# Kernel optimization log

Hardware: AMD Instinct MI355X
Metric: run time of the kernel (lower is better)

## Reference

```python
import jax, jax.numpy as jnp
import numpy as np

B, L, V, D, H, C = 2048, 200, 50000, 300, 128, 20


def setup_inputs() -> dict:
    key = jax.random.key(0)
    k = jax.random.split(key, 7)
    x = jax.random.randint(k[0], (B, L), 0, V)
    lengths = jax.random.randint(k[1], (B,), 1, L + 1)  # avoid div-by-zero
    emb_table = jax.random.normal(k[2], (V, D), dtype=jnp.float32)
    W_new = jax.random.normal(k[3], (H, 2 * D), dtype=jnp.float32) * 0.02
    b_new = jax.random.normal(k[4], (H,), dtype=jnp.float32) * 0.02
    W3 = jax.random.normal(k[5], (C, H), dtype=jnp.float32) * 0.02
    b3 = jax.random.normal(k[6], (C,), dtype=jnp.float32) * 0.02
    return {"x": x, "lengths": lengths, "emb_table": emb_table,
            "W_new": W_new, "b_new": b_new, "W3": W3, "b3": b3}


def reference(x, lengths, emb_table, W_new, b_new, W3, b3):
    # [B, L, D] embedding gather
    emb = emb_table[x]
    len_f = lengths.astype(emb.dtype)[:, None]          # [B, 1]
    s = jnp.sum(emb, axis=1)                            # [B, D]
    mx = jnp.max(emb, axis=1)                           # [B, D] (max over padded length, as in original)
    # Original bug preserved: 'mean' feature is sum / lengths^2 (divided twice)
    mean_bug = s / (len_f * len_f)                      # [B, D]
    rep = jnp.concatenate([mean_bug, mx], axis=-1)      # [B, 2D]
    h = jax.nn.relu(rep @ W_new.T + b_new)              # [B, H]
    logits2 = h @ W3.T + b3                             # [B, C]
    return logits2
```

## Files before the change

### kernel.cpp

```cpp
#include <hip/hip_runtime.h>
#include <math.h>

#define B_ 2048
#define L_ 200
#define V_ 50000
#define D_ 300
#define H_ 128
#define C_ 20

__global__ __launch_bounds__(256, 4) void gather_reduce_kernel(
    const int* __restrict__ x,
    const int* __restrict__ lengths,
    const float* __restrict__ emb,
    float* __restrict__ rep)
{
    __shared__ int s_idx[L_];
    __shared__ float4 s_sum[225];
    __shared__ float4 s_max[225];

    const int b = blockIdx.x;
    const int t = threadIdx.x;

    if (t < L_) s_idx[t] = x[b * L_ + t];
    __syncthreads();

    if (t < 225) {
        const int g = t / 75;
        const int p = t - g * 75;
        float4 s4 = make_float4(0.f, 0.f, 0.f, 0.f);
        float4 m4 = make_float4(-INFINITY, -INFINITY, -INFINITY, -INFINITY);
        #pragma unroll 4
        for (int l = g; l < L_; l += 3) {
            const float4 v =
                *(const float4*)(emb + (size_t)s_idx[l] * D_ + (p << 2));
            s4.x += v.x; s4.y += v.y; s4.z += v.z; s4.w += v.w;
            m4.x = fmaxf(m4.x, v.x); m4.y = fmaxf(m4.y, v.y);
            m4.z = fmaxf(m4.z, v.z); m4.w = fmaxf(m4.w, v.w);
        }
        s_sum[t] = s4;
        s_max[t] = m4;
    }
    __syncthreads();

    if (t < 75) {
        const float4 sa = s_sum[t], sb = s_sum[t + 75], sc = s_sum[t + 150];
        const float4 ma = s_max[t], mb = s_max[t + 75], mc = s_max[t + 150];
        const float lf = (float)lengths[b];
        const float inv = 1.0f / (lf * lf);
        float4 S, M;
        S.x = (sa.x + sb.x + sc.x) * inv;
        S.y = (sa.y + sb.y + sc.y) * inv;
        S.z = (sa.z + sb.z + sc.z) * inv;
        S.w = (sa.w + sb.w + sc.w) * inv;
        M.x = fmaxf(fmaxf(ma.x, mb.x), mc.x);
        M.y = fmaxf(fmaxf(ma.y, mb.y), mc.y);
        M.z = fmaxf(fmaxf(ma.z, mb.z), mc.z);
        M.w = fmaxf(fmaxf(ma.w, mb.w), mc.w);
        float4* o = (float4*)(rep + (size_t)b * (2 * D_));
        o[t]      = S;
        o[75 + t] = M;
    }
}

__global__ __launch_bounds__(256) void mlp8_kernel(
    const float* __restrict__ rep,
    const float* __restrict__ W_new,
    const float* __restrict__ b_new,
    const float* __restrict__ W3,
    const float* __restrict__ b3,
    float* __restrict__ out)
{
    __shared__ float4 s_rep[8][150];
    __shared__ float  s_h[8][H_ + 4];

    const int t = threadIdx.x;
    const int row0 = blockIdx.x * 8;

    {
        const float4* src = (const float4*)(rep + (size_t)row0 * (2 * D_));
        float4* dst = (float4*)&s_rep[0][0];
        #pragma unroll
        for (int i = 0; i < 5; ++i) {
            const int j = t + (i << 8);
            if (j < 1200) dst[j] = src[j];
        }
    }
    __syncthreads();

    const int lane2 = t & 3;
    const int c0 = t >> 2;
    const int c1 = c0 + 64;

    float acc0[8] = {0.f, 0.f, 0.f, 0.f, 0.f, 0.f, 0.f, 0.f};
    float acc1[8] = {0.f, 0.f, 0.f, 0.f, 0.f, 0.f, 0.f, 0.f};

    const float4* w0row = (const float4*)(W_new + (size_t)c0 * (2 * D_));
    const float4* w1row = (const float4*)(W_new + (size_t)c1 * (2 * D_));

    #pragma unroll 2
    for (int i = 0; i < 38; ++i) {
        const int q = lane2 + (i << 2);
        if (q < 150) {
            const float4 w0 = w0row[q];
            const float4 w1 = w1row[q];
            #pragma unroll
            for (int r = 0; r < 8; ++r) {
                const float4 rq = s_rep[r][q];
                acc0[r] = fmaf(w0.x, rq.x, acc0[r]);
                acc0[r] = fmaf(w0.y, rq.y, acc0[r]);
                acc0[r] = fmaf(w0.z, rq.z, acc0[r]);
                acc0[r] = fmaf(w0.w, rq.w, acc0[r]);
                acc1[r] = fmaf(w1.x, rq.x, acc1[r]);
                acc1[r] = fmaf(w1.y, rq.y, acc1[r]);
                acc1[r] = fmaf(w1.z, rq.z, acc1[r]);
                acc1[r] = fmaf(w1.w, rq.w, acc1[r]);
            }
        }
    }

    const float bn0 = b_new[c0];
    const float bn1 = b_new[c1];
    #pragma unroll
    for (int r = 0; r < 8; ++r) {
        float a0 = acc0[r];
        a0 += __shfl_xor(a0, 1);
        a0 += __shfl_xor(a0, 2);
        float a1 = acc1[r];
        a1 += __shfl_xor(a1, 1);
        a1 += __shfl_xor(a1, 2);
        if (lane2 == 0) {
            s_h[r][c0] = fmaxf(a0 + bn0, 0.f);
            s_h[r][c1] = fmaxf(a1 + bn1, 0.f);
        }
    }
    __syncthreads();

    if (t < 8 * C_) {
        const int r = t / C_;
        const int c = t - r * C_;
        const float* hr = s_h[r];
        const float* w3 = W3 + c * H_;
        float acc = b3[c];
        #pragma unroll 8
        for (int k = 0; k < H_; ++k) acc = fmaf(hr[k], w3[k], acc);
        out[(size_t)(row0 + r) * C_ + c] = acc;
    }
}

extern "C" void kernel_launch(void* const* d_in, const int* in_sizes, int n_in,
                              void* d_out, int out_size, void* d_ws, size_t ws_size,
                              hipStream_t stream) {
    const int*   x       = (const int*)  d_in[0];
    const int*   lengths = (const int*)  d_in[1];
    const float* emb     = (const float*)d_in[2];
    const float* W_new   = (const float*)d_in[3];
    const float* b_new   = (const float*)d_in[4];
    const float* W3      = (const float*)d_in[5];
    const float* b3      = (const float*)d_in[6];
    float* out = (float*)d_out;
    float* rep = (float*)d_ws;

    gather_reduce_kernel<<<B_, 256, 0, stream>>>(x, lengths, emb, rep);
    mlp8_kernel<<<B_ / 8, 256, 0, stream>>>(rep, W_new, b_new, W3, b3, out);
}
```

Measured before the change: 180.9 us.

## Fuse gather-reduce and MLP into one kernel via last-block-done atomic counters

Merges the two kernels into one. Each block gathers and reduces one row, then bumps an atomic counter for its group of 8 rows. The last block to finish a group runs the MLP for those 8 rows, which removes the second kernel launch and the kernel boundary. This adds a memset, threadfences and an atomic per block, and the MLP work is now serialized onto the tail blocks. Launch bounds lose the occupancy hint of 4, and the W3 dot-product loop is vectorised to float4.

```diff
diff --git a/kernel.cpp b/kernel.cpp
--- a/kernel.cpp
+++ b/kernel.cpp
@@ -8,20 +8,40 @@
 #define H_ 128
 #define C_ 20
 
-__global__ __launch_bounds__(256, 4) void gather_reduce_kernel(
+#define REP_FLOATS (B_ * 2 * D_)
+#define DONE_OFF   (5u * 1024u * 1024u)
+
+union Smem {
+    struct {
+        int    idx[L_];
+        float4 sum[225];
+        float4 mx[225];
+    } g;
+    struct {
+        float4 rep[8][150];
+        float  h[8][H_ + 4];
+    } m;
+};
+
+__global__ __launch_bounds__(256) void fused_persist_kernel(
     const int* __restrict__ x,
     const int* __restrict__ lengths,
     const float* __restrict__ emb,
-    float* __restrict__ rep)
+    const float* __restrict__ W_new,
+    const float* __restrict__ b_new,
+    const float* __restrict__ W3,
+    const float* __restrict__ b3,
+    float* __restrict__ rep,
+    int* __restrict__ done,
+    float* __restrict__ out)
 {
-    __shared__ int s_idx[L_];
-    __shared__ float4 s_sum[225];
-    __shared__ float4 s_max[225];
+    __shared__ Smem s;
+    __shared__ int s_doer;
 
     const int b = blockIdx.x;
     const int t = threadIdx.x;
 
-    if (t < L_) s_idx[t] = x[b * L_ + t];
+    if (t < L_) s.g.idx[t] = x[b * L_ + t];
     __syncthreads();
 
     if (t < 225) {
@@ -32,19 +52,19 @@
         #pragma unroll 4
         for (int l = g; l < L_; l += 3) {
             const float4 v =
-                *(const float4*)(emb + (size_t)s_idx[l] * D_ + (p << 2));
+                *(const float4*)(emb + (size_t)s.g.idx[l] * D_ + (p << 2));
             s4.x += v.x; s4.y += v.y; s4.z += v.z; s4.w += v.w;
             m4.x = fmaxf(m4.x, v.x); m4.y = fmaxf(m4.y, v.y);
             m4.z = fmaxf(m4.z, v.z); m4.w = fmaxf(m4.w, v.w);
         }
-        s_sum[t] = s4;
-        s_max[t] = m4;
+        s.g.sum[t] = s4;
+        s.g.mx[t]  = m4;
     }
     __syncthreads();
 
     if (t < 75) {
-        const float4 sa = s_sum[t], sb = s_sum[t + 75], sc = s_sum[t + 150];
-        const float4 ma = s_max[t], mb = s_max[t + 75], mc = s_max[t + 150];
+        const float4 sa = s.g.sum[t], sb = s.g.sum[t + 75], sc = s.g.sum[t + 150];
+        const float4 ma = s.g.mx[t],  mb = s.g.mx[t + 75],  mc = s.g.mx[t + 150];
         const float lf = (float)lengths[b];
         const float inv = 1.0f / (lf * lf);
         float4 S, M;
@@ -60,25 +80,23 @@
         o[t]      = S;
         o[75 + t] = M;
     }
-}
+    __syncthreads();
 
-__global__ __launch_bounds__(256) void mlp8_kernel(
-    const float* __restrict__ rep,
-    const float* __restrict__ W_new,
-    const float* __restrict__ b_new,
-    const float* __restrict__ W3,
-    const float* __restrict__ b3,
-    float* __restrict__ out)
-{
-    __shared__ float4 s_rep[8][150];
-    __shared__ float  s_h[8][H_ + 4];
+    if (t == 0) {
+        __threadfence();
+        const int old = atomicAdd(&done[b >> 3], 1);
+        s_doer = (old == 7) ? 1 : 0;
+    }
+    __syncthreads();
+    if (!s_doer) return;
+    if (t == 0) __threadfence();
+    __syncthreads();
 
-    const int t = threadIdx.x;
-    const int row0 = blockIdx.x * 8;
+    const int row0 = (b >> 3) * 8;
 
     {
         const float4* src = (const float4*)(rep + (size_t)row0 * (2 * D_));
-        float4* dst = (float4*)&s_rep[0][0];
+        float4* dst = &s.m.rep[0][0];
         #pragma unroll
         for (int i = 0; i < 5; ++i) {
             const int j = t + (i << 8);
@@ -101,19 +119,19 @@
     for (int i = 0; i < 38; ++i) {
         const int q = lane2 + (i << 2);
         if (q < 150) {
-            const float4 w0 = w0row[q];
-            const float4 w1 = w1row[q];
+            const float4 wa = w0row[q];
+            const float4 wb = w1row[q];
             #pragma unroll
             for (int r = 0; r < 8; ++r) {
-                const float4 rq = s_rep[r][q];
-                acc0[r] = fmaf(w0.x, rq.x, acc0[r]);
-                acc0[r] = fmaf(w0.y, rq.y, acc0[r]);
-                acc0[r] = fmaf(w0.z, rq.z, acc0[r]);
-                acc0[r] = fmaf(w0.w, rq.w, acc0[r]);
-                acc1[r] = fmaf(w1.x, rq.x, acc1[r]);
-                acc1[r] = fmaf(w1.y, rq.y, acc1[r]);
-                acc1[r] = fmaf(w1.z, rq.z, acc1[r]);
-                acc1[r] = fmaf(w1.w, rq.w, acc1[r]);
+                const float4 rq = s.m.rep[r][q];
+                acc0[r] = fmaf(wa.x, rq.x, acc0[r]);
+                acc0[r] = fmaf(wa.y, rq.y, acc0[r]);
+                acc0[r] = fmaf(wa.z, rq.z, acc0[r]);
+                acc0[r] = fmaf(wa.w, rq.w, acc0[r]);
+                acc1[r] = fmaf(wb.x, rq.x, acc1[r]);
+                acc1[r] = fmaf(wb.y, rq.y, acc1[r]);
+                acc1[r] = fmaf(wb.z, rq.z, acc1[r]);
+                acc1[r] = fmaf(wb.w, rq.w, acc1[r]);
             }
         }
     }
@@ -129,21 +147,28 @@
         a1 += __shfl_xor(a1, 1);
         a1 += __shfl_xor(a1, 2);
         if (lane2 == 0) {
-            s_h[r][c0] = fmaxf(a0 + bn0, 0.f);
-            s_h[r][c1] = fmaxf(a1 + bn1, 0.f);
+            s.m.h[r][c0] = fmaxf(a0 + bn0, 0.f);
+            s.m.h[r][c1] = fmaxf(a1 + bn1, 0.f);
         }
     }
     __syncthreads();
 
     if (t < 8 * C_) {
         const int r = t / C_;
-        const int c = t - r * C_;
-        const float* hr = s_h[r];
-        const float* w3 = W3 + c * H_;
-        float acc = b3[c];
+        const int cc = t - r * C_;
+        const float4* w3 = (const float4*)(W3 + cc * H_);
+        const float4* h4 = (const float4*)&s.m.h[r][0];
+        float acc2 = b3[cc];
         #pragma unroll 8
-        for (int k = 0; k < H_; ++k) acc = fmaf(hr[k], w3[k], acc);
-        out[(size_t)(row0 + r) * C_ + c] = acc;
+        for (int k = 0; k < 32; ++k) {
+            const float4 wv = w3[k];
+            const float4 hv = h4[k];
+            acc2 = fmaf(hv.x, wv.x, acc2);
+            acc2 = fmaf(hv.y, wv.y, acc2);
+            acc2 = fmaf(hv.z, wv.z, acc2);
+            acc2 = fmaf(hv.w, wv.w, acc2);
+        }
+        out[(size_t)(row0 + r) * C_ + cc] = acc2;
     }
 }
 
@@ -157,9 +182,12 @@
     const float* b_new   = (const float*)d_in[4];
     const float* W3      = (const float*)d_in[5];
     const float* b3      = (const float*)d_in[6];
-    float* out = (float*)d_out;
-    float* rep = (float*)d_ws;
+    float* out  = (float*)d_out;
+    float* rep  = (float*)d_ws;
+    int*   done = (int*)((char*)d_ws + DONE_OFF);
 
-    gather_reduce_kernel<<<B_, 256, 0, stream>>>(x, lengths, emb, rep);
-    mlp8_kernel<<<B_ / 8, 256, 0, stream>>>(rep, W_new, b_new, W3, b3, out);
+    hipMemsetAsync(done, 0, 256 * sizeof(int), stream);
+
+    fused_persist_kernel<<<B_, 256, 0, stream>>>(
+        x, lengths, emb, W_new, b_new, W3, b3, rep, done, out);
 }
```

Measured after the change: 284.7 us. 1.57x slower.
